# Kernel optimization log

Measured on AMD Instinct MI355X. Metric: run time of the kernel, lower is better.

## Reference

```python
import jax, jax.numpy as jnp
import numpy as np

B, E, T, H = 2, 1024, 2048, 16
DH = E // H


def _conv1x1(x, W, b, mask):
    # x: [B,C,T], W: [O,C], b: [O], mask: [B,1,T] (norm=False -> plain conv on masked input)
    x = x * mask
    return jnp.einsum('oc,bct->bot', W, x) + b[None, :, None]


def setup_inputs() -> dict:
    key = jax.random.key(0)
    ks = jax.random.split(key, 16)
    inp = {
        'q': jax.random.normal(ks[0], (B, E, T), jnp.float32),
        'k': jax.random.normal(ks[1], (B, E, T), jnp.float32),
        'v': jax.random.normal(ks[2], (B, E, T), jnp.float32),
        'query_mask': (jax.random.uniform(ks[3], (B, 1, T)) < 0.9).astype(jnp.float32),
        'key_mask': (jax.random.uniform(ks[4], (B, 1, T)) < 0.9).astype(jnp.float32),
        'value_mask': (jax.random.uniform(ks[5], (B, 1, T)) < 0.9).astype(jnp.float32),
        'Wq': jax.random.normal(ks[6], (E, E), jnp.float32) * (1.0 / np.sqrt(E)),
        'bq': jnp.zeros((E,), jnp.float32),
        'Wk': jax.random.normal(ks[7], (E, E), jnp.float32) * (1.0 / np.sqrt(E)),
        'bk': jnp.zeros((E,), jnp.float32),
        'Wv': jax.random.normal(ks[8], (E, E), jnp.float32) * (1.0 / np.sqrt(E)),
        'bv': jnp.zeros((E,), jnp.float32),
        'Wo': jax.random.normal(ks[9], (E, E), jnp.float32) * (1.0 / np.sqrt(E)),
        'bo': jnp.zeros((E,), jnp.float32),
    }
    return inp


def reference(q, k, v, query_mask, key_mask, value_mask, Wq, bq, Wk, bk, Wv, bv, Wo, bo):
    # 1x1 conv projections with input masking (norm=False path)
    qp = _conv1x1(q, Wq, bq, query_mask)   # [B,E,T]
    kp = _conv1x1(k, Wk, bk, key_mask)
    vp = _conv1x1(v, Wv, bv, value_mask)
    # split heads: [B,E,T] -> [B,H,DH,T]
    qh = qp.reshape(B, H, DH, T)
    kh = kp.reshape(B, H, DH, T)
    vh = vp.reshape(B, H, DH, T)
    # scores = q^T k with pre-softmax multiplicative masks, scaled by sqrt(embed_dim)
    scores = jnp.einsum('bhdq,bhdk->bhqk', qh, kh)
    scores = scores * query_mask[:, :, :, None] * key_mask[:, :, None, :] / np.sqrt(E)
    attn = jax.nn.softmax(scores, axis=-1) * key_mask[:, :, None, :]  # post-softmax mask
    # transpose_scores=False path: v @ scores (contracts v's time dim with the query dim)
    out = jnp.einsum('bhdq,bhqk->bhdk', vh, attn)  # [B,H,DH,T]
    out = out.reshape(B, E, T)
    return _conv1x1(out, Wo, bo, key_mask)
```

## Files before the change

### kernel.cpp

```cpp
#include <hip/hip_runtime.h>

#define B 2
#define E 1024
#define T 2048
#define H 16
#define DH 64

#define SCALE2 0.0450842200277801f

typedef _Float16 f16x8 __attribute__((ext_vector_type(8)));
typedef float f32x4 __attribute__((ext_vector_type(4)));
typedef float f32x16 __attribute__((ext_vector_type(16)));
typedef unsigned short ushort8v __attribute__((ext_vector_type(8)));
typedef unsigned int uint4v __attribute__((ext_vector_type(4)));

__device__ __forceinline__ f32x4 mfma16(f16x8 a, f16x8 b, f32x4 c) {
  return __builtin_amdgcn_mfma_f32_16x16x32_f16(a, b, c, 0, 0, 0);
}
__device__ __forceinline__ f32x16 mfma32(f16x8 a, f16x8 b, f32x16 c) {
  return __builtin_amdgcn_mfma_f32_32x32x16_f16(a, b, c, 0, 0, 0);
}
__device__ __forceinline__ unsigned short f16u(float x) {
  _Float16 h = (_Float16)x;
  return __builtin_bit_cast(unsigned short, h);
}
__device__ __forceinline__ float ex2(float x) {
  return __builtin_amdgcn_exp2f(x);
}
__device__ __forceinline__ unsigned int pk16(float a, float b) {
  auto h = __builtin_amdgcn_cvt_pkrtz(a, b);
  return __builtin_bit_cast(unsigned int, h);
}
__device__ __forceinline__ void plswap(unsigned int& a, unsigned int& b) {
  auto r = __builtin_amdgcn_permlane32_swap(a, b, false, false);
  a = r[0];
  b = r[1];
}

__global__ __launch_bounds__(256) void prep_weights(
    const float* __restrict__ Wq, const float* __restrict__ Wk,
    const float* __restrict__ Wv, const float* __restrict__ Wo,
    unsigned short* __restrict__ WqB, unsigned short* __restrict__ WkB,
    unsigned short* __restrict__ WvB, unsigned short* __restrict__ WoB) {
  const int which = blockIdx.y;
  const int i = (blockIdx.x * 256 + threadIdx.x) * 4;
  const float* src = which == 0 ? Wq : which == 1 ? Wk : which == 2 ? Wv : Wo;
  unsigned short* dst = which == 0 ? WqB : which == 1 ? WkB : which == 2 ? WvB : WoB;
  float4 v = *(const float4*)&src[i];
  ((unsigned int*)&dst[i])[0] = f16u(v.x) | ((unsigned)f16u(v.y) << 16);
  ((unsigned int*)&dst[i])[1] = f16u(v.z) | ((unsigned)f16u(v.w) << 16);
}

__global__ __launch_bounds__(256) void transpose_cvt(
    const float* __restrict__ q, const float* __restrict__ k,
    const float* __restrict__ v, unsigned short* __restrict__ XtQ,
    unsigned short* __restrict__ XtK, unsigned short* __restrict__ XtV) {
  __shared__ float Xs[32 * 36];
  const int z = blockIdx.z, which = z >> 1, b = z & 1;
  const float* X = which == 0 ? q : which == 1 ? k : v;
  unsigned short* O = which == 0 ? XtQ : which == 1 ? XtK : XtV;
  const int e0 = blockIdx.y * 32, t0 = blockIdx.x * 32;
  const int tid = threadIdx.x;
  const int r = tid >> 3, c = (tid & 7) * 4;
  *(float4*)&Xs[r * 36 + c] = *(const float4*)&X[((size_t)b * E + e0 + r) * T + t0 + c];
  __syncthreads();
  unsigned short h[4];
#pragma unroll
  for (int j = 0; j < 4; ++j) h[j] = f16u(Xs[(c + j) * 36 + r]);
  const size_t o = ((size_t)b * T + t0 + r) * E + e0 + c;
  ((unsigned int*)&O[o])[0] = h[0] | ((unsigned)h[1] << 16);
  ((unsigned int*)&O[o])[1] = h[2] | ((unsigned)h[3] << 16);
}

__global__ __launch_bounds__(256) void proj_qkv(
    const unsigned short* __restrict__ WqB, const unsigned short* __restrict__ WkB,
    const unsigned short* __restrict__ WvB, const unsigned short* __restrict__ XtQ,
    const unsigned short* __restrict__ XtK, const unsigned short* __restrict__ XtV,
    const float* __restrict__ bq, const float* __restrict__ bk,
    const float* __restrict__ bv, const float* __restrict__ qmask,
    const float* __restrict__ kmask, const float* __restrict__ vmask,
    unsigned short* __restrict__ qp2, unsigned short* __restrict__ kp2,
    unsigned short* __restrict__ vp) {
  __shared__ unsigned short Ah[128 * 72], Bs[128 * 72];
  const int b = blockIdx.z, my = blockIdx.y;
  const int which = my >> 3, o0 = (my & 7) * 128, t0 = blockIdx.x * 128;
  const unsigned short* W = which == 0 ? WqB : which == 1 ? WkB : WvB;
  const unsigned short* Xt = which == 0 ? XtQ : which == 1 ? XtK : XtV;
  const float* bias = which == 0 ? bq : which == 1 ? bk : bv;
  const float* mask = which == 0 ? qmask : which == 1 ? kmask : vmask;

  const int tid = threadIdx.x, wave = tid >> 6, lane = tid & 63;
  const int lg = lane & 15, quad = lane >> 4;
  const int wm = (wave & 1) * 64, wn = (wave >> 1) * 64;
  const int sr = tid >> 3, sc = (tid & 7) * 8;

  f32x4 acc[4][4];
#pragma unroll
  for (int i = 0; i < 4; ++i)
#pragma unroll
    for (int j = 0; j < 4; ++j) acc[i][j] = (f32x4){0.f, 0.f, 0.f, 0.f};

  for (int k0 = 0; k0 < E; k0 += 64) {
    ushort8v ra[4], rb[4];
#pragma unroll
    for (int p = 0; p < 4; ++p) {
      ra[p] = *(const ushort8v*)&W[(size_t)(o0 + p * 32 + sr) * E + k0 + sc];
      rb[p] = *(const ushort8v*)&Xt[((size_t)b * T + t0 + p * 32 + sr) * E + k0 + sc];
    }
    __syncthreads();
#pragma unroll
    for (int p = 0; p < 4; ++p) {
      *(ushort8v*)&Ah[(p * 32 + sr) * 72 + sc] = ra[p];
      *(ushort8v*)&Bs[(p * 32 + sr) * 72 + sc] = rb[p];
    }
    __syncthreads();
    f16x8 af[4][2];
#pragma unroll
    for (int mt = 0; mt < 4; ++mt) {
      af[mt][0] = *(const f16x8*)&Ah[(wm + mt * 16 + lg) * 72 + quad * 8];
      af[mt][1] = *(const f16x8*)&Ah[(wm + mt * 16 + lg) * 72 + 32 + quad * 8];
    }
#pragma unroll
    for (int nt = 0; nt < 4; ++nt) {
      f16x8 b0 = *(const f16x8*)&Bs[(wn + nt * 16 + lg) * 72 + quad * 8];
      f16x8 b1 = *(const f16x8*)&Bs[(wn + nt * 16 + lg) * 72 + 32 + quad * 8];
#pragma unroll
      for (int mt = 0; mt < 4; ++mt) {
        f32x4 c = acc[mt][nt];
        c = mfma16(af[mt][0], b0, c);
        c = mfma16(af[mt][1], b1, c);
        acc[mt][nt] = c;
      }
    }
  }
#pragma unroll
  for (int nt = 0; nt < 4; ++nt) {
    const int tcol = t0 + wn + nt * 16 + lg;
    const float mv = mask[b * T + tcol];
#pragma unroll
    for (int mt = 0; mt < 4; ++mt) {
      const int oF = o0 + wm + mt * 16 + quad * 4;
      float v4[4];
      if (which == 0) {
        const float s = mv * SCALE2;
#pragma unroll
        for (int r = 0; r < 4; ++r) v4[r] = (acc[mt][nt][r] + bias[oF + r]) * s;
      } else if (which == 1) {
#pragma unroll
        for (int r = 0; r < 4; ++r) v4[r] = (acc[mt][nt][r] + bias[oF + r]) * mv;
      } else {
#pragma unroll
        for (int r = 0; r < 4; ++r) v4[r] = acc[mt][nt][r] * mv + bias[oF + r];
      }
      if (which <= 1) {
        unsigned short* O = which == 0 ? qp2 : kp2;
        const int head = (o0 + wm) >> 6;
        const int bh2 = b * H + head;
        const size_t idx8 =
            (((size_t)(bh2 * (T / 32) + (tcol >> 5)) * 4 + mt) * 32 + (tcol & 31)) * 2 +
            (quad >> 1);
        unsigned int* dst = (unsigned int*)(O + idx8 * 8 + (quad & 1) * 4);
        dst[0] = f16u(v4[0]) | ((unsigned)f16u(v4[1]) << 16);
        dst[1] = f16u(v4[2]) | ((unsigned)f16u(v4[3]) << 16);
      } else {
#pragma unroll
        for (int r = 0; r < 4; ++r)
          vp[((size_t)b * E + oF + r) * T + tcol] = f16u(v4[r]);
      }
    }
  }
}

__global__ __launch_bounds__(256) void repack_v(
    const unsigned short* __restrict__ vp, unsigned short* __restrict__ vp2) {
  __shared__ unsigned short Ls[64 * 136];
  const int q0 = blockIdx.x * 128, hh = blockIdx.y, b = blockIdx.z;
  const int bh = b * H + hh;
  const int tid = threadIdx.x;
#pragma unroll
  for (int w = 0; w < 2; ++w) {
    const int d = w * 32 + (tid >> 3);
    const int c = (tid & 7) * 16;
    const unsigned short* src = vp + ((size_t)b * E + hh * DH + d) * T + q0 + c;
    *(ushort8v*)&Ls[d * 136 + c] = *(const ushort8v*)src;
    *(ushort8v*)&Ls[d * 136 + c + 8] = *(const ushort8v*)(src + 8);
  }
  __syncthreads();
#pragma unroll
  for (int w = 0; w < 4; ++w) {
    const int flat = w * 256 + tid;
    const int hb = flat & 1, lnv = (flat >> 1) & 31, dt = (flat >> 6) & 1,
              qgl = flat >> 7;
    ushort8v val = *(const ushort8v*)&Ls[(dt * 32 + lnv) * 136 + qgl * 16 + hb * 8];
    const size_t idx8 =
        (((size_t)(bh * (T / 16) + (q0 >> 4) + qgl) * 2 + dt) * 32 + lnv) * 2 + hb;
    *(ushort8v*)&vp2[idx8 * 8] = val;
  }
}

__global__ __launch_bounds__(256) void attn_stats(
    const unsigned short* __restrict__ qp2, const unsigned short* __restrict__ kp2,
    float* __restrict__ sPart) {
  const int bh = blockIdx.y;
  const int z = blockIdx.z;
  const int q0 = blockIdx.x * 128;
  const int tid = threadIdx.x, wave = tid >> 6, lane = tid & 63;
  const int ln = lane & 31, half = lane >> 5;

  const int t32q = (q0 >> 5) + wave;
  f16x8 aq[4];
#pragma unroll
  for (int s = 0; s < 4; ++s)
    aq[s] = *(const f16x8*)&qp2[((((size_t)bh * (T / 32) + t32q) * 4 + s) * 64 +
                                 ln * 2 + half) * 8];

  float lacc[16];
#pragma unroll
  for (int r = 0; r < 16; ++r) lacc[r] = 0.f;

  const int kbase = z * (T / 2);
  const int kend = kbase + T / 2;

  const unsigned short* pk0 =
      kp2 + (((size_t)bh * (T / 32) + (kbase >> 5)) * 4) * 512 + (ln * 2 + half) * 8;
  const unsigned short* pk1 = pk0 + 2048;

  f16x8 bkr[2][4];
#pragma unroll
  for (int s = 0; s < 4; ++s) {
    bkr[0][s] = *(const f16x8*)(pk0 + s * 512);
    bkr[1][s] = *(const f16x8*)(pk1 + s * 512);
  }
  pk0 += 4096;
  pk1 += 4096;

  for (int kt = kbase; kt < kend; kt += 64) {
    f16x8 nb[2][4];
#pragma unroll
    for (int s = 0; s < 4; ++s) {
      nb[0][s] = *(const f16x8*)(pk0 + s * 512);
      nb[1][s] = *(const f16x8*)(pk1 + s * 512);
    }
    pk0 += 4096;
    pk1 += 4096;
    f32x16 S0 = {}, S1 = {};
#pragma unroll
    for (int s = 0; s < 4; ++s) {
      S0 = mfma32(aq[s], bkr[0][s], S0);
      S1 = mfma32(aq[s], bkr[1][s], S1);
    }
#pragma unroll
    for (int r = 0; r < 16; ++r) lacc[r] += ex2(S0[r]) + ex2(S1[r]);
#pragma unroll
    for (int nt = 0; nt < 2; ++nt)
#pragma unroll
      for (int s = 0; s < 4; ++s) bkr[nt][s] = nb[nt][s];
  }
#pragma unroll
  for (int off = 1; off < 32; off <<= 1)
#pragma unroll
    for (int r = 0; r < 16; ++r) lacc[r] += __shfl_xor(lacc[r], off, 64);
  if (ln == 0) {
#pragma unroll
    for (int t = 0; t < 4; ++t) {
      f32x4 o;
#pragma unroll
      for (int j = 0; j < 4; ++j) o[j] = lacc[t * 4 + j];
      *(f32x4*)&sPart[((size_t)z * (B * H) + bh) * T + q0 + wave * 32 + t * 8 +
                      half * 4] = o;
    }
  }
}

__global__ __launch_bounds__(256) void stats_merge(
    const float* __restrict__ sPart, float* __restrict__ lLog) {
  const int i = (blockIdx.x * 256 + threadIdx.x) * 4;
  const int N = B * H * T;
  f32x4 a = *(const f32x4*)&sPart[i];
  f32x4 b = *(const f32x4*)&sPart[N + i];
  f32x4 o;
#pragma unroll
  for (int j = 0; j < 4; ++j) o[j] = -__builtin_amdgcn_logf(a[j] + b[j]);
  *(f32x4*)&lLog[i] = o;
}

#define APPLY_LOAD(AQ, AV, LL)                                                        \
  {                                                                                   \
    _Pragma("unroll") for (int s = 0; s < 4; ++s) AQ[s] =                             \
        *(const f16x8*)(pq + s * 512);                                                \
    _Pragma("unroll") for (int dt = 0; dt < 2; ++dt)                                  \
        _Pragma("unroll") for (int f = 0; f < 2; ++f) AV[dt][f] =                     \
        *(const f16x8*)(pv + dt * 512 + f * 1024);                                    \
    _Pragma("unroll") for (int t = 0; t < 4; ++t) LL[t] =                             \
        *(const f32x4*)(pl + t * 8);                                                  \
    pq += 2048;                                                                       \
    pv += 2048;                                                                       \
    pl += 32;                                                                         \
  }

#define APPLY_COMPUTE(AQ, AV, LL)                                                     \
  {                                                                                   \
    f32x16 S0, S1;                                                                    \
    _Pragma("unroll") for (int r = 0; r < 16; ++r) {                                  \
      const float c_ = LL[r >> 2][r & 3];                                             \
      S0[r] = c_;                                                                     \
      S1[r] = c_;                                                                     \
    }                                                                                 \
    _Pragma("unroll") for (int s = 0; s < 4; ++s) S0 = mfma32(AQ[s], bkk[0][s], S0);  \
    _Pragma("unroll") for (int s = 0; s < 4; ++s) S1 = mfma32(AQ[s], bkk[1][s], S1);  \
    {                                                                                 \
      unsigned int w[8];                                                              \
      _Pragma("unroll") for (int p = 0; p < 8; ++p)                                   \
          w[p] = pk16(ex2(S0[p * 2 + 0]), ex2(S0[p * 2 + 1]));                        \
      plswap(w[0], w[2]); plswap(w[1], w[3]);                                         \
      plswap(w[4], w[6]); plswap(w[5], w[7]);                                         \
      uint4v f0v, f1v;                                                                \
      f0v[0] = w[0]; f0v[1] = w[1]; f0v[2] = w[2]; f0v[3] = w[3];                     \
      f1v[0] = w[4]; f1v[1] = w[5]; f1v[2] = w[6]; f1v[3] = w[7];                     \
      const f16x8 pf0 = __builtin_bit_cast(f16x8, f0v);                               \
      const f16x8 pf1 = __builtin_bit_cast(f16x8, f1v);                               \
      acc00 = mfma32(AV[0][0], pf0, acc00);                                           \
      acc00 = mfma32(AV[0][1], pf1, acc00);                                           \
      acc01 = mfma32(AV[1][0], pf0, acc01);                                           \
      acc01 = mfma32(AV[1][1], pf1, acc01);                                           \
    }                                                                                 \
    {                                                                                 \
      unsigned int w[8];                                                              \
      _Pragma("unroll") for (int p = 0; p < 8; ++p)                                   \
          w[p] = pk16(ex2(S1[p * 2 + 0]), ex2(S1[p * 2 + 1]));                        \
      plswap(w[0], w[2]); plswap(w[1], w[3]);                                         \
      plswap(w[4], w[6]); plswap(w[5], w[7]);                                         \
      uint4v f0v, f1v;                                                                \
      f0v[0] = w[0]; f0v[1] = w[1]; f0v[2] = w[2]; f0v[3] = w[3];                     \
      f1v[0] = w[4]; f1v[1] = w[5]; f1v[2] = w[6]; f1v[3] = w[7];                     \
      const f16x8 pf0 = __builtin_bit_cast(f16x8, f0v);                               \
      const f16x8 pf1 = __builtin_bit_cast(f16x8, f1v);                               \
      acc10 = mfma32(AV[0][0], pf0, acc10);                                           \
      acc10 = mfma32(AV[0][1], pf1, acc10);                                           \
      acc11 = mfma32(AV[1][0], pf0, acc11);                                           \
      acc11 = mfma32(AV[1][1], pf1, acc11);                                           \
    }                                                                                 \
  }

__global__ __launch_bounds__(256) void attn_apply(
    const unsigned short* __restrict__ qp2, const unsigned short* __restrict__ kp2,
    const unsigned short* __restrict__ vp2, const float* __restrict__ lLog,
    unsigned short* __restrict__ ao) {
  __shared__ float st[64 * 130];
  const int bh = blockIdx.y, b = bh >> 4, h = bh & 15;
  const int kblk = blockIdx.x * 128;
  const int tid = threadIdx.x, wave = tid >> 6, lane = tid & 63;
  const int ln = lane & 31, half = lane >> 5;
  const int kt = wave & 1, qh = wave >> 1;

  const int t32k = (kblk >> 5) + kt * 2;
  f16x8 bkk[2][4];
#pragma unroll
  for (int sub = 0; sub < 2; ++sub)
#pragma unroll
    for (int s = 0; s < 4; ++s)
      bkk[sub][s] = *(const f16x8*)&kp2[((((size_t)bh * (T / 32) + t32k + sub) * 4 + s) *
                                             64 + ln * 2 + half) * 8];

  f32x16 acc00 = {}, acc01 = {}, acc10 = {}, acc11 = {};
  const int qstart = qh * (T / 2);
  const int qend = qstart + T / 2;

  const unsigned short* pq =
      qp2 + (((size_t)bh * (T / 32) + (qstart >> 5)) * 4) * 512 + (ln * 2 + half) * 8;
  const unsigned short* pv =
      vp2 + ((size_t)bh * (T / 16) + (qstart >> 4)) * 1024 + ln * 16 + half * 8;
  const float* pl = lLog + (size_t)bh * T + qstart + half * 4;

  f16x8 aqX[4], avX[2][2], aqY[4], avY[2][2];
  f32x4 llX[4], llY[4];
  APPLY_LOAD(aqX, avX, llX)

  for (int qt = qstart; qt < qend; qt += 64) {
    APPLY_LOAD(aqY, avY, llY)
    APPLY_COMPUTE(aqX, avX, llX)
    APPLY_LOAD(aqX, avX, llX)
    APPLY_COMPUTE(aqY, avY, llY)
  }

  __syncthreads();
  if (qh == 1) {
#pragma unroll
    for (int i = 0; i < 16; ++i) {
      st[(0 * 16 + i) * 130 + kt * 65 + lane] = acc00[i];
      st[(1 * 16 + i) * 130 + kt * 65 + lane] = acc01[i];
      st[(2 * 16 + i) * 130 + kt * 65 + lane] = acc10[i];
      st[(3 * 16 + i) * 130 + kt * 65 + lane] = acc11[i];
    }
  }
  __syncthreads();
  if (qh == 0) {
#pragma unroll
    for (int i = 0; i < 16; ++i) {
      acc00[i] += st[(0 * 16 + i) * 130 + kt * 65 + lane];
      acc01[i] += st[(1 * 16 + i) * 130 + kt * 65 + lane];
      acc10[i] += st[(2 * 16 + i) * 130 + kt * 65 + lane];
      acc11[i] += st[(3 * 16 + i) * 130 + kt * 65 + lane];
    }
#pragma unroll
    for (int sub = 0; sub < 2; ++sub) {
      const int kcol = kblk + kt * 64 + sub * 32 + ln;
      const size_t obase = ((size_t)b * T + kcol) * E + h * DH;
#pragma unroll
      for (int dt = 0; dt < 2; ++dt) {
        const float* a = sub == 0 ? (dt ? (const float*)&acc01 : (const float*)&acc00)
                                  : (dt ? (const float*)&acc11 : (const float*)&acc10);
#pragma unroll
        for (int t = 0; t < 4; ++t) {
          uint2 wv;
          wv.x = f16u(a[t * 4 + 0]) | ((unsigned)f16u(a[t * 4 + 1]) << 16);
          wv.y = f16u(a[t * 4 + 2]) | ((unsigned)f16u(a[t * 4 + 3]) << 16);
          *(uint2*)&ao[obase + dt * 32 + t * 8 + half * 4] = wv;
        }
      }
    }
  }
}

__global__ __launch_bounds__(256) void proj_final(
    const unsigned short* __restrict__ WoB, const unsigned short* __restrict__ ao,
    const float* __restrict__ bo, const float* __restrict__ kmask,
    float* __restrict__ out) {
  __shared__ unsigned short As[64 * 68], Bs[128 * 68];
  const int b = blockIdx.z, o0 = blockIdx.y * 64, t0 = blockIdx.x * 128;
  const int tid = threadIdx.x, wave = tid >> 6, lane = tid & 63;
  const int ln = lane & 31, half = lane >> 5;
  const int wn = wave * 32;
  const int ar = tid >> 2, ac = (tid & 3) * 16;
  const int br = tid >> 1, bc = (tid & 1) * 32;

  f32x16 acc0 = {}, acc1 = {};

  for (int k0 = 0; k0 < E; k0 += 64) {
    ushort8v a0 = *(const ushort8v*)&WoB[(size_t)(o0 + ar) * E + k0 + ac];
    ushort8v a1 = *(const ushort8v*)&WoB[(size_t)(o0 + ar) * E + k0 + ac + 8];
    ushort8v b0 = *(const ushort8v*)&ao[((size_t)b * T + t0 + br) * E + k0 + bc];
    ushort8v b1 = *(const ushort8v*)&ao[((size_t)b * T + t0 + br) * E + k0 + bc + 8];
    ushort8v b2 = *(const ushort8v*)&ao[((size_t)b * T + t0 + br) * E + k0 + bc + 16];
    ushort8v b3 = *(const ushort8v*)&ao[((size_t)b * T + t0 + br) * E + k0 + bc + 24];
    __syncthreads();
    *(ushort8v*)&As[ar * 68 + ac] = a0;
    *(ushort8v*)&As[ar * 68 + ac + 8] = a1;
    *(ushort8v*)&Bs[br * 68 + bc] = b0;
    *(ushort8v*)&Bs[br * 68 + bc + 8] = b1;
    *(ushort8v*)&Bs[br * 68 + bc + 16] = b2;
    *(ushort8v*)&Bs[br * 68 + bc + 24] = b3;
    __syncthreads();
#pragma unroll
    for (int s = 0; s < 4; ++s) {
      f16x8 af0 = *(const f16x8*)&As[ln * 68 + s * 16 + half * 8];
      f16x8 af1 = *(const f16x8*)&As[(32 + ln) * 68 + s * 16 + half * 8];
      f16x8 bf = *(const f16x8*)&Bs[(wn + ln) * 68 + s * 16 + half * 8];
      acc0 = mfma32(af0, bf, acc0);
      acc1 = mfma32(af1, bf, acc1);
    }
  }
  const int tcol = t0 + wn + ln;
  const float mv = kmask[b * T + tcol];
#pragma unroll
  for (int dt = 0; dt < 2; ++dt) {
    const float* a = dt ? (const float*)&acc1 : (const float*)&acc0;
#pragma unroll
    for (int t = 0; t < 4; ++t)
#pragma unroll
      for (int j = 0; j < 4; ++j) {
        const int e = o0 + dt * 32 + t * 8 + half * 4 + j;
        out[((size_t)b * E + e) * T + tcol] = a[t * 4 + j] * mv + bo[e];
      }
  }
}

extern "C" void kernel_launch(void* const* d_in, const int* in_sizes, int n_in,
                              void* d_out, int out_size, void* d_ws, size_t ws_size,
                              hipStream_t stream) {
  const float* q = (const float*)d_in[0];
  const float* k = (const float*)d_in[1];
  const float* v = (const float*)d_in[2];
  const float* qmask = (const float*)d_in[3];
  const float* kmask = (const float*)d_in[4];
  const float* vmask = (const float*)d_in[5];
  const float* Wq = (const float*)d_in[6];
  const float* bq = (const float*)d_in[7];
  const float* Wk = (const float*)d_in[8];
  const float* bk = (const float*)d_in[9];
  const float* Wv = (const float*)d_in[10];
  const float* bv = (const float*)d_in[11];
  const float* Wo = (const float*)d_in[12];
  const float* bo = (const float*)d_in[13];

  char* w = (char*)d_ws;
  const size_t WB = (size_t)E * E * sizeof(unsigned short);
  const size_t TB = (size_t)B * T * E * sizeof(unsigned short);
  unsigned short* WqB = (unsigned short*)(w + 0 * WB);
  unsigned short* WkB = (unsigned short*)(w + 1 * WB);
  unsigned short* WvB = (unsigned short*)(w + 2 * WB);
  unsigned short* WoB = (unsigned short*)(w + 3 * WB);
  size_t off = 4 * WB;
  unsigned short* XtQ = (unsigned short*)(w + off); off += TB;
  unsigned short* qp2 = (unsigned short*)(w + off); off += TB;
  unsigned short* kp2 = (unsigned short*)(w + off); off += TB;
  unsigned short* vp2 = (unsigned short*)(w + off); off += TB;
  float* lLog = (float*)(w + off); off += (size_t)B * H * T * sizeof(float);
  float* sPart = (float*)(w + off); off += (size_t)2 * B * H * T * sizeof(float);
  unsigned short* XtK = (unsigned short*)(w + off); off += TB;
  unsigned short* XtV = (unsigned short*)(w + off); off += TB;
  unsigned short* vp  = (unsigned short*)(w + off); off += TB;
  unsigned short* ao = XtQ;

  dim3 bl(256);
  prep_weights<<<dim3((E * E) / 1024, 4), bl, 0, stream>>>(
      Wq, Wk, Wv, Wo, WqB, WkB, WvB, WoB);
  transpose_cvt<<<dim3(T / 32, E / 32, 3 * B), bl, 0, stream>>>(
      q, k, v, XtQ, XtK, XtV);
  proj_qkv<<<dim3(T / 128, 24, B), bl, 0, stream>>>(
      WqB, WkB, WvB, XtQ, XtK, XtV, bq, bk, bv, qmask, kmask, vmask, qp2, kp2, vp);
  repack_v<<<dim3(T / 128, H, B), bl, 0, stream>>>(vp, vp2);
  attn_stats<<<dim3(T / 128, B * H, 2), bl, 0, stream>>>(qp2, kp2, sPart);
  stats_merge<<<dim3((B * H * T) / 1024), bl, 0, stream>>>(sPart, lLog);
  attn_apply<<<dim3(T / 128, B * H), bl, 0, stream>>>(qp2, kp2, vp2, lLog, ao);
  proj_final<<<dim3(T / 128, E / 64, B), bl, 0, stream>>>(
      WoB, ao, bo, kmask, (float*)d_out);
}
```

Baseline: 259.8 us.

## Fuse V repack into projection epilogue and remap attn_apply block order

The V projection epilogue now writes straight into the MFMA-friendly vp2 layout, so the separate repack_v kernel and the intermediate vp buffer go away. This removes one launch and a full read and write of the V tensor. In exchange, the epilogue does scattered 2-byte stores. attn_apply also moves to a 1D grid whose index places blocks of different heads near each other, probably to spread work across XCDs or L2.

```diff
diff --git a/kernel.cpp b/kernel.cpp
--- a/kernel.cpp
+++ b/kernel.cpp
@@ -80,7 +80,7 @@
     const float* __restrict__ bv, const float* __restrict__ qmask,
     const float* __restrict__ kmask, const float* __restrict__ vmask,
     unsigned short* __restrict__ qp2, unsigned short* __restrict__ kp2,
-    unsigned short* __restrict__ vp) {
+    unsigned short* __restrict__ vp2) {
   __shared__ unsigned short Ah[128 * 72], Bs[128 * 72];
   const int b = blockIdx.z, my = blockIdx.y;
   const int which = my >> 3, o0 = (my & 7) * 128, t0 = blockIdx.x * 128;
@@ -163,38 +163,17 @@
         dst[0] = f16u(v4[0]) | ((unsigned)f16u(v4[1]) << 16);
         dst[1] = f16u(v4[2]) | ((unsigned)f16u(v4[3]) << 16);
       } else {
-#pragma unroll
-        for (int r = 0; r < 4; ++r)
-          vp[((size_t)b * E + oF + r) * T + tcol] = f16u(v4[r]);
+        const int head = (o0 + wm) >> 6;
+        const int bh2 = b * H + head;
+        const size_t qbase =
+            ((size_t)(bh2 * (T / 16) + (tcol >> 4))) * 1024 + (tcol & 15);
+#pragma unroll
+        for (int r = 0; r < 4; ++r) {
+          const int hd = (oF + r) & 63;
+          vp2[qbase + ((size_t)(hd >> 5) * 32 + (hd & 31)) * 16] = f16u(v4[r]);
+        }
       }
     }
-  }
-}
-
-__global__ __launch_bounds__(256) void repack_v(
-    const unsigned short* __restrict__ vp, unsigned short* __restrict__ vp2) {
-  __shared__ unsigned short Ls[64 * 136];
-  const int q0 = blockIdx.x * 128, hh = blockIdx.y, b = blockIdx.z;
-  const int bh = b * H + hh;
-  const int tid = threadIdx.x;
-#pragma unroll
-  for (int w = 0; w < 2; ++w) {
-    const int d = w * 32 + (tid >> 3);
-    const int c = (tid & 7) * 16;
-    const unsigned short* src = vp + ((size_t)b * E + hh * DH + d) * T + q0 + c;
-    *(ushort8v*)&Ls[d * 136 + c] = *(const ushort8v*)src;
-    *(ushort8v*)&Ls[d * 136 + c + 8] = *(const ushort8v*)(src + 8);
-  }
-  __syncthreads();
-#pragma unroll
-  for (int w = 0; w < 4; ++w) {
-    const int flat = w * 256 + tid;
-    const int hb = flat & 1, lnv = (flat >> 1) & 31, dt = (flat >> 6) & 1,
-              qgl = flat >> 7;
-    ushort8v val = *(const ushort8v*)&Ls[(dt * 32 + lnv) * 136 + qgl * 16 + hb * 8];
-    const size_t idx8 =
-        (((size_t)(bh * (T / 16) + (q0 >> 4) + qgl) * 2 + dt) * 32 + lnv) * 2 + hb;
-    *(ushort8v*)&vp2[idx8 * 8] = val;
   }
 }
 
@@ -347,8 +326,11 @@
     const unsigned short* __restrict__ vp2, const float* __restrict__ lLog,
     unsigned short* __restrict__ ao) {
   __shared__ float st[64 * 130];
-  const int bh = blockIdx.y, b = bh >> 4, h = bh & 15;
-  const int kblk = blockIdx.x * 128;
+  const int n = blockIdx.x;
+  const int s_ = n >> 3;
+  const int bh = (n & 7) * 4 + (s_ >> 4);
+  const int kblk = (s_ & 15) * 128;
+  const int b = bh >> 4, h = bh & 15;
   const int tid = threadIdx.x, wave = tid >> 6, lane = tid & 63;
   const int ln = lane & 31, half = lane >> 5;
   const int kt = wave & 1, qh = wave >> 1;
@@ -509,7 +491,6 @@
   float* sPart = (float*)(w + off); off += (size_t)2 * B * H * T * sizeof(float);
   unsigned short* XtK = (unsigned short*)(w + off); off += TB;
   unsigned short* XtV = (unsigned short*)(w + off); off += TB;
-  unsigned short* vp  = (unsigned short*)(w + off); off += TB;
   unsigned short* ao = XtQ;
 
   dim3 bl(256);
@@ -518,11 +499,10 @@
   transpose_cvt<<<dim3(T / 32, E / 32, 3 * B), bl, 0, stream>>>(
       q, k, v, XtQ, XtK, XtV);
   proj_qkv<<<dim3(T / 128, 24, B), bl, 0, stream>>>(
-      WqB, WkB, WvB, XtQ, XtK, XtV, bq, bk, bv, qmask, kmask, vmask, qp2, kp2, vp);
-  repack_v<<<dim3(T / 128, H, B), bl, 0, stream>>>(vp, vp2);
+      WqB, WkB, WvB, XtQ, XtK, XtV, bq, bk, bv, qmask, kmask, vmask, qp2, kp2, vp2);
   attn_stats<<<dim3(T / 128, B * H, 2), bl, 0, stream>>>(qp2, kp2, sPart);
   stats_merge<<<dim3((B * H * T) / 1024), bl, 0, stream>>>(sPart, lLog);
-  attn_apply<<<dim3(T / 128, B * H), bl, 0, stream>>>(qp2, kp2, vp2, lLog, ao);
+  attn_apply<<<dim3(512), bl, 0, stream>>>(qp2, kp2, vp2, lLog, ao);
   proj_final<<<dim3(T / 128, E / 64, B), bl, 0, stream>>>(
       WoB, ao, bo, kmask, (float*)d_out);
 }
```

New measurement: 256.0 us, median of 3. About the same (-1.5%).
